# Kernel tuning notes

Measured on AMD Instinct MI355X. Metric: run time of the kernel, lower is better.

The kernel has to match this reference:

```python
import jax, jax.numpy as jnp
import numpy as np

N_NODES = 50000
N_EDGES = 400000
IN_CH = 7
EMBED = 128
EDGE_DIM = 6


def setup_inputs() -> dict:
    key = jax.random.key(0)
    ks = jax.random.split(key, 10)
    x = jax.random.normal(ks[0], (N_NODES, IN_CH), dtype=jnp.float32)
    edge_index = jax.random.randint(ks[1], (2, N_EDGES), 0, N_NODES, dtype=jnp.int64)
    edge_attr = jax.random.normal(ks[2], (N_EDGES, EDGE_DIM), dtype=jnp.float32)
    # edge MLP params: Linear(6,128) -> GELU -> Linear(128, 7*128)
    s1 = 1.0 / np.sqrt(EDGE_DIM)
    s2 = 1.0 / np.sqrt(EMBED)
    W1 = jax.random.uniform(ks[3], (EDGE_DIM, EMBED), jnp.float32, -s1, s1)
    b1 = jax.random.uniform(ks[4], (EMBED,), jnp.float32, -s1, s1)
    W2 = jax.random.uniform(ks[5], (EMBED, IN_CH * EMBED), jnp.float32, -s2, s2)
    b2 = jax.random.uniform(ks[6], (IN_CH * EMBED,), jnp.float32, -s2, s2)
    # NNConv root weight and bias
    s3 = 1.0 / np.sqrt(IN_CH)
    root = jax.random.uniform(ks[7], (IN_CH, EMBED), jnp.float32, -s3, s3)
    bias = jnp.zeros((EMBED,), dtype=jnp.float32)
    return {"x": x, "edge_index": edge_index, "edge_attr": edge_attr,
            "W1": W1, "b1": b1, "W2": W2, "b2": b2, "root": root, "bias": bias}


def reference(x, edge_index, edge_attr, W1, b1, W2, b2, root, bias):
    N = x.shape[0]
    src, dst = edge_index[0], edge_index[1]
    # edge MLP -> per-edge weight matrix [E, in_ch, embed]
    h = jax.nn.gelu(edge_attr @ W1 + b1, approximate=False)
    w = (h @ W2 + b2).reshape(-1, IN_CH, EMBED)
    # gather source node features, per-edge small matmul
    msg = jnp.einsum('ei,eio->eo', x[src], w)  # [E, embed]
    # mean aggregation at target nodes
    summed = jax.ops.segment_sum(msg, dst, num_segments=N)
    cnt = jax.ops.segment_sum(jnp.ones((msg.shape[0],), msg.dtype), dst, num_segments=N)
    aggr = summed / jnp.clip(cnt, 1.0)[:, None]
    return aggr + x @ root + bias
```

## Files before the change

kernel.cpp:

```cpp
#include <hip/hip_runtime.h>
#include <stdint.h>

#define NNODES 50000
#define NEDGES 400000
#define EMB 128
#define KD 896
#define BM 128

typedef __attribute__((ext_vector_type(8))) short bf16x8;
typedef __attribute__((ext_vector_type(4))) float f32x4;

__device__ __forceinline__ short f2bf(float f) {
  union { float f; uint32_t u; } v; v.f = f;
  uint32_t r = v.u + 0x7FFFu + ((v.u >> 16) & 1u);
  return (short)(r >> 16);
}
__device__ __forceinline__ float bf2f(short s) {
  union { uint32_t u; float f; } v; v.u = ((uint32_t)(uint16_t)s) << 16;
  return v.f;
}
__device__ __forceinline__ float fast_gelu(float x) {
  float x2 = x * x;
  float y = x * (0.7978845608f + 0.03567740814f * x2);
  float e = __expf(2.0f * y);
  float r = __builtin_amdgcn_rcpf(1.0f + e);
  return x - x * r;
}

__global__ void prep_B(const float* __restrict__ W2, short* __restrict__ Bp) {
  int idx = blockIdx.x * 256 + threadIdx.x;
  int m = idx & 7, l = (idx >> 3) & 63, c = idx >> 9;
  int sidx = c >> 2, wn = (c >> 1) & 1, f = c & 1;
  int p = sidx >> 2, kk = sidx & 3, i = p >> 1, fnh = p & 1;
  int o = (wn * 4 + fnh * 2 + f) * 16 + (l & 15);
  int k = kk * 32 + (l >> 4) * 8 + m;
  Bp[idx] = f2bf(W2[k * KD + i * EMB + o]);
}

__global__ void prep_W1(const float* __restrict__ W1f, const float* __restrict__ b1,
                        short* __restrict__ W1p) {
  int idx = blockIdx.x * 256 + threadIdx.x;
  int m = idx & 7, l = (idx >> 3) & 63, mt = idx >> 9;
  int o = mt * 16 + (l & 15), kseg = l >> 4;
  short v = 0;
  if (kseg < 2) {
    if (m < 6) v = f2bf(W1f[m * EMB + o]);
  } else if (kseg == 2) {
    if (m < 6) { float wv = W1f[m * EMB + o]; short hi = f2bf(wv); v = f2bf(wv - bf2f(hi)); }
  } else {
    if (m == 0) v = f2bf(b1[o]);
    else if (m == 1) { float bv = b1[o]; short hi = f2bf(bv); v = f2bf(bv - bf2f(hi)); }
  }
  W1p[idx] = v;
}

__global__ __launch_bounds__(256, 2)
void nnconv_main(const float* __restrict__ x,
                 const int* __restrict__ ei,
                 const float* __restrict__ ea,
                 const float* __restrict__ b2,
                 const short* __restrict__ Bp,
                 const short* __restrict__ W1p,
                 float* __restrict__ cnt,
                 float* __restrict__ out) {
  __shared__ __align__(16) short h_s[BM * EMB];
  __shared__ __align__(16) float x_t[7][132];
  __shared__ __align__(16) float ea_s[BM * 6];
  __shared__ int dst_s[BM];

  const int t = threadIdx.x;
  const int lane = t & 63;
  const int w = t >> 6;
  const int wm = w >> 1, wn = w & 1;
  const int rowA = lane & 15;
  const int kseg = lane >> 4;
  const int eb = blockIdx.x * BM;
  const char* BpB = (const char*)Bp + wn * 2048 + lane * 16;

  bf16x8 bcur[4][2];
#pragma unroll
  for (int kk = 0; kk < 4; ++kk)
#pragma unroll
    for (int f = 0; f < 2; ++f)
      bcur[kk][f] = *(const bf16x8*)(BpB + (((size_t)kk * 4 + f) << 10));

  if (t < 192)
    *(float4*)&ea_s[t * 4] = *(const float4*)&ea[(size_t)eb * 6 + t * 4];
  if (t < BM) {
    int s = ei[eb + t];
    int d = ei[NEDGES + eb + t];
    dst_s[t] = d;
#pragma unroll
    for (int i = 0; i < 7; ++i) x_t[i][t] = x[s * 7 + i];
    atomicAdd(&cnt[d], 1.0f);
  }
  __syncthreads();

  {
    bf16x8 wa[8];
#pragma unroll
    for (int mt = 0; mt < 8; ++mt)
      wa[mt] = *(const bf16x8*)(W1p + (mt * 64 + lane) * 8);
#pragma unroll
    for (int et2 = 0; et2 < 2; ++et2) {
      const int e = w * 32 + et2 * 16 + rowA;
      bf16x8 be = (bf16x8){0, 0, 0, 0, 0, 0, 0, 0};
      if (kseg == 3) {
        be[0] = f2bf(1.0f); be[1] = f2bf(1.0f);
      } else {
#pragma unroll
        for (int q = 0; q < 6; ++q) {
          float v = ea_s[e * 6 + q];
          short hi = f2bf(v);
          be[q] = (kseg == 1) ? f2bf(v - bf2f(hi)) : hi;
        }
      }
      const int swz = (e & 15) << 4;
#pragma unroll
      for (int mt = 0; mt < 8; ++mt) {
        f32x4 d = __builtin_amdgcn_mfma_f32_16x16x32_bf16(
            wa[mt], be, (f32x4){0.f, 0.f, 0.f, 0.f}, 0, 0, 0);
        uint32_t h0 = (uint16_t)f2bf(fast_gelu(d[0]));
        uint32_t h1 = (uint16_t)f2bf(fast_gelu(d[1]));
        uint32_t h2 = (uint16_t)f2bf(fast_gelu(d[2]));
        uint32_t h3 = (uint16_t)f2bf(fast_gelu(d[3]));
        uint2 u; u.x = h0 | (h1 << 16); u.y = h2 | (h3 << 16);
        int off = (mt * 32 + kseg * 8) ^ swz;
        *(uint2*)((char*)h_s + e * 256 + off) = u;
      }
    }
  }
  __syncthreads();

  bf16x8 A[4][4];
#pragma unroll
  for (int kk = 0; kk < 4; ++kk)
#pragma unroll
    for (int fm = 0; fm < 4; ++fm) {
      int row = wm * 64 + fm * 16 + rowA;
      int off = (kk * 64 + kseg * 16) ^ (rowA << 4);
      A[kk][fm] = *(const bf16x8*)((const char*)h_s + row * 256 + off);
    }

#pragma unroll
  for (int fh = 0; fh < 2; ++fh) {
    f32x4 acc2[4][2];
#pragma unroll
    for (int a = 0; a < 4; ++a) {
      acc2[a][0] = (f32x4){0.f, 0.f, 0.f, 0.f};
      acc2[a][1] = (f32x4){0.f, 0.f, 0.f, 0.f};
    }
#pragma unroll 1
    for (int i = 0; i < 7; ++i) {
      float b2v0 = b2[i * EMB + wn * 64 + fh * 32 + rowA];
      float b2v1 = b2[i * EMB + wn * 64 + fh * 32 + 16 + rowA];
      int nsidx;
      if (fh == 0) nsidx = (i < 6) ? (i + 1) * 8 : 4;
      else         nsidx = (i < 6) ? (i + 1) * 8 + 4 : 52;

      f32x4 tmp[4][2];
      const f32x4 zz = (f32x4){0.f, 0.f, 0.f, 0.f};
#pragma unroll
      for (int fm = 0; fm < 4; ++fm) {
        tmp[fm][0] = __builtin_amdgcn_mfma_f32_16x16x32_bf16(A[0][fm], bcur[0][0], zz, 0, 0, 0);
        tmp[fm][1] = __builtin_amdgcn_mfma_f32_16x16x32_bf16(A[0][fm], bcur[0][1], zz, 0, 0, 0);
      }
      bcur[0][0] = *(const bf16x8*)(BpB + (((size_t)(nsidx + 0) * 4 + 0) << 10));
      bcur[0][1] = *(const bf16x8*)(BpB + (((size_t)(nsidx + 0) * 4 + 1) << 10));
#pragma unroll
      for (int kk = 1; kk < 4; ++kk) {
#pragma unroll
        for (int fm = 0; fm < 4; ++fm) {
          tmp[fm][0] = __builtin_amdgcn_mfma_f32_16x16x32_bf16(A[kk][fm], bcur[kk][0], tmp[fm][0], 0, 0, 0);
          tmp[fm][1] = __builtin_amdgcn_mfma_f32_16x16x32_bf16(A[kk][fm], bcur[kk][1], tmp[fm][1], 0, 0, 0);
        }
        bcur[kk][0] = *(const bf16x8*)(BpB + (((size_t)(nsidx + kk) * 4 + 0) << 10));
        bcur[kk][1] = *(const bf16x8*)(BpB + (((size_t)(nsidx + kk) * 4 + 1) << 10));
      }
#pragma unroll
      for (int fm = 0; fm < 4; ++fm) {
        f32x4 xv = *(const f32x4*)&x_t[i][wm * 64 + fm * 16 + kseg * 4];
#pragma unroll
        for (int r = 0; r < 4; ++r) {
          acc2[fm][0][r] += xv[r] * (tmp[fm][0][r] + b2v0);
          acc2[fm][1][r] += xv[r] * (tmp[fm][1][r] + b2v1);
        }
      }
    }
#pragma unroll
    for (int fm = 0; fm < 4; ++fm)
#pragma unroll
      for (int r = 0; r < 4; ++r) {
        const int row = wm * 64 + fm * 16 + kseg * 4 + r;
        const int d = dst_s[row];
        float* op = out + (size_t)d * EMB + wn * 64 + fh * 32 + rowA;
        atomicAdd(op, acc2[fm][0][r]);
        atomicAdd(op + 16, acc2[fm][1][r]);
      }
  }
}

__global__ void finalize(const float* __restrict__ x, const float* __restrict__ root,
                         const float* __restrict__ bias, const float* __restrict__ cnt,
                         float* __restrict__ out) {
  int idx = blockIdx.x * 256 + threadIdx.x;
  int n = idx >> 7, o = idx & 127;
  float c = fmaxf(cnt[n], 1.0f);
  float v = out[idx] / c + bias[o];
#pragma unroll
  for (int i = 0; i < 7; ++i) v += x[n * 7 + i] * root[i * EMB + o];
  out[idx] = v;
}

extern "C" void kernel_launch(void* const* d_in, const int* in_sizes, int n_in,
                              void* d_out, int out_size, void* d_ws, size_t ws_size,
                              hipStream_t stream) {
  const float* x    = (const float*)d_in[0];
  const int*   ei   = (const int*)d_in[1];
  const float* ea   = (const float*)d_in[2];
  const float* W1   = (const float*)d_in[3];
  const float* b1   = (const float*)d_in[4];
  const float* W2   = (const float*)d_in[5];
  const float* b2   = (const float*)d_in[6];
  const float* root = (const float*)d_in[7];
  const float* bias = (const float*)d_in[8];
  float* out = (float*)d_out;

  short* Bp  = (short*)d_ws;
  short* W1p = (short*)((char*)d_ws + 128 * KD * 2);
  float* cnt = (float*)((char*)d_ws + 128 * KD * 2 + 8192);

  hipMemsetAsync(out, 0, (size_t)NNODES * EMB * sizeof(float), stream);
  hipMemsetAsync(cnt, 0, (size_t)NNODES * sizeof(float), stream);
  prep_B<<<448, 256, 0, stream>>>(W2, Bp);
  prep_W1<<<16, 256, 0, stream>>>(W1, b1, W1p);
  nnconv_main<<<NEDGES / BM, 256, 0, stream>>>(x, ei, ea, b2, Bp, W1p, cnt, out);
  finalize<<<NNODES * EMB / 256, 256, 0, stream>>>(x, root, bias, cnt, out);
}
```

Before: 301.3 us.

## Sort edges by destination and reduce runs in LDS before output atomics

Adds a counting sort of edges by destination node (histogram, single-block scan, scatter) so each main-kernel tile processes edges grouped by destination. Per-edge messages are staged in shared memory and each wave sums consecutive same-destination rows, issuing a plain store for runs fully inside its 32-row segment and an atomic only at segment boundaries. This cuts global float atomics roughly by the average in-degree. The cost is three extra kernel launches, a serial single-block scan, an extra LDS round trip, and gathered (uncoalesced) edge_attr and edge_index reads through the permutation.

```diff
diff --git a/kernel.cpp b/kernel.cpp
--- a/kernel.cpp
+++ b/kernel.cpp
@@ -54,6 +54,40 @@
   W1p[idx] = v;
 }
 
+__global__ void hist_dst(const int* __restrict__ ei, unsigned* __restrict__ cnt) {
+  int e = blockIdx.x * 256 + threadIdx.x;
+  if (e < NEDGES) atomicAdd(&cnt[ei[NEDGES + e]], 1u);
+}
+
+__global__ __launch_bounds__(1024)
+void scan_off(const unsigned* __restrict__ cnt, unsigned* __restrict__ woff) {
+  __shared__ unsigned ps[1024];
+  const int t = threadIdx.x;
+  const int lo = t * 49;
+  const int hi = (lo + 49 < NNODES) ? lo + 49 : NNODES;
+  unsigned s = 0;
+  for (int j = lo; j < hi; ++j) s += cnt[j];
+  ps[t] = s;
+  __syncthreads();
+  for (int d = 1; d < 1024; d <<= 1) {
+    unsigned v = (t >= d) ? ps[t - d] : 0u;
+    __syncthreads();
+    ps[t] += v;
+    __syncthreads();
+  }
+  unsigned run = (t > 0) ? ps[t - 1] : 0u;
+  for (int j = lo; j < hi; ++j) { woff[j] = run; run += cnt[j]; }
+}
+
+__global__ void scatter_e(const int* __restrict__ ei, unsigned* __restrict__ woff,
+                          unsigned* __restrict__ eord) {
+  int e = blockIdx.x * 256 + threadIdx.x;
+  if (e < NEDGES) {
+    unsigned p = atomicAdd(&woff[ei[NEDGES + e]], 1u);
+    eord[p] = (unsigned)e;
+  }
+}
+
 __global__ __launch_bounds__(256, 2)
 void nnconv_main(const float* __restrict__ x,
                  const int* __restrict__ ei,
@@ -61,12 +95,14 @@
                  const float* __restrict__ b2,
                  const short* __restrict__ Bp,
                  const short* __restrict__ W1p,
-                 float* __restrict__ cnt,
+                 const unsigned* __restrict__ eord,
                  float* __restrict__ out) {
-  __shared__ __align__(16) short h_s[BM * EMB];
+  __shared__ __align__(16) char smem[33280];
+  short* h_s = (short*)smem;
+  float* red_s = (float*)smem;
   __shared__ __align__(16) float x_t[7][132];
   __shared__ __align__(16) float ea_s[BM * 6];
-  __shared__ int dst_s[BM];
+  __shared__ int dst_s[BM + 4];
 
   const int t = threadIdx.x;
   const int lane = t & 63;
@@ -84,16 +120,17 @@
     for (int f = 0; f < 2; ++f)
       bcur[kk][f] = *(const bf16x8*)(BpB + (((size_t)kk * 4 + f) << 10));
 
-  if (t < 192)
-    *(float4*)&ea_s[t * 4] = *(const float4*)&ea[(size_t)eb * 6 + t * 4];
   if (t < BM) {
-    int s = ei[eb + t];
-    int d = ei[NEDGES + eb + t];
+    const int e = (int)eord[eb + t];
+    const int s = ei[e];
+    const int d = ei[NEDGES + e];
     dst_s[t] = d;
 #pragma unroll
     for (int i = 0; i < 7; ++i) x_t[i][t] = x[s * 7 + i];
-    atomicAdd(&cnt[d], 1.0f);
-  }
+#pragma unroll
+    for (int q = 0; q < 6; ++q) ea_s[t * 6 + q] = ea[(size_t)e * 6 + q];
+  }
+  if (t == BM) dst_s[BM] = -1;
   __syncthreads();
 
   {
@@ -187,25 +224,44 @@
         }
       }
     }
+
+    __syncthreads();
 #pragma unroll
     for (int fm = 0; fm < 4; ++fm)
 #pragma unroll
       for (int r = 0; r < 4; ++r) {
         const int row = wm * 64 + fm * 16 + kseg * 4 + r;
-        const int d = dst_s[row];
-        float* op = out + (size_t)d * EMB + wn * 64 + fh * 32 + rowA;
-        atomicAdd(op, acc2[fm][0][r]);
-        atomicAdd(op + 16, acc2[fm][1][r]);
-      }
+        red_s[row * 65 + wn * 32 + rowA]      = acc2[fm][0][r];
+        red_s[row * 65 + wn * 32 + 16 + rowA] = acc2[fm][1][r];
+      }
+    __syncthreads();
+    {
+      const int gcol = fh * 32 + (lane & 31) + (lane >> 5) * 64;
+      const int base = w * 32;
+      float run = 0.f;
+      int runstart = 0;
+      for (int j = 0; j < 32; ++j) {
+        run += red_s[(base + j) * 65 + lane];
+        const int d = dst_s[base + j];
+        const bool endrun = (j == 31) || (dst_s[base + j + 1] != d);
+        if (endrun) {
+          float* op = out + (size_t)d * EMB + gcol;
+          if (runstart > 0 && j < 31) *op = run;
+          else atomicAdd(op, run);
+          run = 0.f;
+          runstart = j + 1;
+        }
+      }
+    }
   }
 }
 
 __global__ void finalize(const float* __restrict__ x, const float* __restrict__ root,
-                         const float* __restrict__ bias, const float* __restrict__ cnt,
+                         const float* __restrict__ bias, const unsigned* __restrict__ cnt,
                          float* __restrict__ out) {
   int idx = blockIdx.x * 256 + threadIdx.x;
   int n = idx >> 7, o = idx & 127;
-  float c = fmaxf(cnt[n], 1.0f);
+  float c = fmaxf((float)cnt[n], 1.0f);
   float v = out[idx] / c + bias[o];
 #pragma unroll
   for (int i = 0; i < 7; ++i) v += x[n * 7 + i] * root[i * EMB + o];
@@ -226,14 +282,19 @@
   const float* bias = (const float*)d_in[8];
   float* out = (float*)d_out;
 
-  short* Bp  = (short*)d_ws;
-  short* W1p = (short*)((char*)d_ws + 128 * KD * 2);
-  float* cnt = (float*)((char*)d_ws + 128 * KD * 2 + 8192);
+  short*    Bp    = (short*)d_ws;
+  short*    W1p   = (short*)((char*)d_ws + 229376);
+  unsigned* cnt_u = (unsigned*)((char*)d_ws + 237568);
+  unsigned* woff  = (unsigned*)((char*)d_ws + 437568);
+  unsigned* eord  = (unsigned*)((char*)d_ws + 637568);
 
   hipMemsetAsync(out, 0, (size_t)NNODES * EMB * sizeof(float), stream);
-  hipMemsetAsync(cnt, 0, (size_t)NNODES * sizeof(float), stream);
+  hipMemsetAsync(cnt_u, 0, (size_t)NNODES * sizeof(unsigned), stream);
   prep_B<<<448, 256, 0, stream>>>(W2, Bp);
   prep_W1<<<16, 256, 0, stream>>>(W1, b1, W1p);
-  nnconv_main<<<NEDGES / BM, 256, 0, stream>>>(x, ei, ea, b2, Bp, W1p, cnt, out);
-  finalize<<<NNODES * EMB / 256, 256, 0, stream>>>(x, root, bias, cnt, out);
-}
+  hist_dst<<<(NEDGES + 255) / 256, 256, 0, stream>>>(ei, cnt_u);
+  scan_off<<<1, 1024, 0, stream>>>(cnt_u, woff);
+  scatter_e<<<(NEDGES + 255) / 256, 256, 0, stream>>>(ei, woff, eord);
+  nnconv_main<<<NEDGES / BM, 256, 0, stream>>>(x, ei, ea, b2, Bp, W1p, eord, out);
+  finalize<<<NNODES * EMB / 256, 256, 0, stream>>>(x, root, bias, cnt_u, out);
+}
```

New measurement: 355.8 us. +18.1%, slower.

## Sort edges by destination and reduce runs before scattering atomics

Applied to the files above, without the earlier changes.

Adds a counting sort of edges by destination: a histogram, a three-kernel prefix scan and a scatter. The main kernel then processes edges in sorted order, stages accumulators through shared memory, and sums runs of equal destinations so most output writes become plain stores. The b2 bias term is factored out through per-node sums of source features and applied in finalize. The main loop also double-buffers the W2 fragment loads. This targets the cost of 128 float atomics per edge, at the price of several extra small kernels, added atomics in the histogram, and an indirect gather of edge attributes.

```diff
diff --git a/kernel.cpp b/kernel.cpp
--- a/kernel.cpp
+++ b/kernel.cpp
@@ -54,19 +54,77 @@
   W1p[idx] = v;
 }
 
+__global__ void hist_dst(const int* __restrict__ ei, const float* __restrict__ x,
+                         unsigned* __restrict__ cnt, float* __restrict__ xsum) {
+  int e = blockIdx.x * 256 + threadIdx.x;
+  if (e < NEDGES) {
+    int d = ei[NEDGES + e];
+    int s = ei[e];
+    atomicAdd(&cnt[d], 1u);
+#pragma unroll
+    for (int i = 0; i < 7; ++i) atomicAdd(&xsum[d * 8 + i], x[s * 7 + i]);
+  }
+}
+
+__global__ void scanA(const unsigned* __restrict__ cnt, unsigned* __restrict__ woff,
+                      unsigned* __restrict__ part) {
+  __shared__ unsigned ps[256];
+  int t = threadIdx.x, n = blockIdx.x * 256 + t;
+  unsigned v = (n < NNODES) ? cnt[n] : 0u;
+  ps[t] = v; __syncthreads();
+  for (int d = 1; d < 256; d <<= 1) {
+    unsigned u = (t >= d) ? ps[t - d] : 0u;
+    __syncthreads(); ps[t] += u; __syncthreads();
+  }
+  if (n < NNODES) woff[n] = ps[t] - v;
+  if (t == 255) part[blockIdx.x] = ps[t];
+}
+
+__global__ void scanB(unsigned* __restrict__ part) {
+  __shared__ unsigned ps[256];
+  int t = threadIdx.x;
+  unsigned v = (t < 196) ? part[t] : 0u;
+  ps[t] = v; __syncthreads();
+  for (int d = 1; d < 256; d <<= 1) {
+    unsigned u = (t >= d) ? ps[t - d] : 0u;
+    __syncthreads(); ps[t] += u; __syncthreads();
+  }
+  if (t < 196) part[t] = ps[t] - v;
+}
+
+__global__ void scanC(unsigned* __restrict__ woff, const unsigned* __restrict__ part) {
+  int n = blockIdx.x * 256 + threadIdx.x;
+  if (n < NNODES) woff[n] += part[blockIdx.x];
+}
+
+__global__ void scatter_e(const int* __restrict__ ei, unsigned* __restrict__ woff,
+                          unsigned* __restrict__ eord, int* __restrict__ dsts,
+                          int* __restrict__ srcs) {
+  int e = blockIdx.x * 256 + threadIdx.x;
+  if (e < NEDGES) {
+    int d = ei[NEDGES + e];
+    unsigned p = atomicAdd(&woff[d], 1u);
+    eord[p] = (unsigned)e;
+    dsts[p] = d;
+    srcs[p] = ei[e];
+  }
+}
+
 __global__ __launch_bounds__(256, 2)
 void nnconv_main(const float* __restrict__ x,
-                 const int* __restrict__ ei,
                  const float* __restrict__ ea,
-                 const float* __restrict__ b2,
                  const short* __restrict__ Bp,
                  const short* __restrict__ W1p,
-                 float* __restrict__ cnt,
+                 const unsigned* __restrict__ eord,
+                 const int* __restrict__ dsts,
+                 const int* __restrict__ srcs,
                  float* __restrict__ out) {
-  __shared__ __align__(16) short h_s[BM * EMB];
+  __shared__ __align__(16) char smem[33280];
+  short* h_s = (short*)smem;
+  float* red_s = (float*)smem;
   __shared__ __align__(16) float x_t[7][132];
   __shared__ __align__(16) float ea_s[BM * 6];
-  __shared__ int dst_s[BM];
+  __shared__ int dst_s[BM + 4];
 
   const int t = threadIdx.x;
   const int lane = t & 63;
@@ -77,23 +135,23 @@
   const int eb = blockIdx.x * BM;
   const char* BpB = (const char*)Bp + wn * 2048 + lane * 16;
 
-  bf16x8 bcur[4][2];
+  bf16x8 bufA[4][2], bufB[4][2];
 #pragma unroll
   for (int kk = 0; kk < 4; ++kk)
 #pragma unroll
     for (int f = 0; f < 2; ++f)
-      bcur[kk][f] = *(const bf16x8*)(BpB + (((size_t)kk * 4 + f) << 10));
-
-  if (t < 192)
-    *(float4*)&ea_s[t * 4] = *(const float4*)&ea[(size_t)eb * 6 + t * 4];
+      bufA[kk][f] = *(const bf16x8*)(BpB + (((size_t)kk * 4 + f) << 10));
+
   if (t < BM) {
-    int s = ei[eb + t];
-    int d = ei[NEDGES + eb + t];
-    dst_s[t] = d;
+    const int s = srcs[eb + t];
+    dst_s[t] = dsts[eb + t];
 #pragma unroll
     for (int i = 0; i < 7; ++i) x_t[i][t] = x[s * 7 + i];
-    atomicAdd(&cnt[d], 1.0f);
-  }
+    const int e = (int)eord[eb + t];
+#pragma unroll
+    for (int q = 0; q < 6; ++q) ea_s[t * 6 + q] = ea[(size_t)e * 6 + q];
+  }
+  if (t == BM) dst_s[BM] = -1;
   __syncthreads();
 
   {
@@ -142,71 +200,109 @@
       A[kk][fm] = *(const bf16x8*)((const char*)h_s + row * 256 + off);
     }
 
-#pragma unroll
-  for (int fh = 0; fh < 2; ++fh) {
-    f32x4 acc2[4][2];
-#pragma unroll
-    for (int a = 0; a < 4; ++a) {
-      acc2[a][0] = (f32x4){0.f, 0.f, 0.f, 0.f};
-      acc2[a][1] = (f32x4){0.f, 0.f, 0.f, 0.f};
-    }
-#pragma unroll 1
-    for (int i = 0; i < 7; ++i) {
-      float b2v0 = b2[i * EMB + wn * 64 + fh * 32 + rowA];
-      float b2v1 = b2[i * EMB + wn * 64 + fh * 32 + 16 + rowA];
-      int nsidx;
-      if (fh == 0) nsidx = (i < 6) ? (i + 1) * 8 : 4;
-      else         nsidx = (i < 6) ? (i + 1) * 8 + 4 : 52;
-
-      f32x4 tmp[4][2];
-      const f32x4 zz = (f32x4){0.f, 0.f, 0.f, 0.f};
-#pragma unroll
-      for (int fm = 0; fm < 4; ++fm) {
-        tmp[fm][0] = __builtin_amdgcn_mfma_f32_16x16x32_bf16(A[0][fm], bcur[0][0], zz, 0, 0, 0);
-        tmp[fm][1] = __builtin_amdgcn_mfma_f32_16x16x32_bf16(A[0][fm], bcur[0][1], zz, 0, 0, 0);
-      }
-      bcur[0][0] = *(const bf16x8*)(BpB + (((size_t)(nsidx + 0) * 4 + 0) << 10));
-      bcur[0][1] = *(const bf16x8*)(BpB + (((size_t)(nsidx + 0) * 4 + 1) << 10));
-#pragma unroll
-      for (int kk = 1; kk < 4; ++kk) {
-#pragma unroll
-        for (int fm = 0; fm < 4; ++fm) {
-          tmp[fm][0] = __builtin_amdgcn_mfma_f32_16x16x32_bf16(A[kk][fm], bcur[kk][0], tmp[fm][0], 0, 0, 0);
-          tmp[fm][1] = __builtin_amdgcn_mfma_f32_16x16x32_bf16(A[kk][fm], bcur[kk][1], tmp[fm][1], 0, 0, 0);
-        }
-        bcur[kk][0] = *(const bf16x8*)(BpB + (((size_t)(nsidx + kk) * 4 + 0) << 10));
-        bcur[kk][1] = *(const bf16x8*)(BpB + (((size_t)(nsidx + kk) * 4 + 1) << 10));
-      }
-#pragma unroll
-      for (int fm = 0; fm < 4; ++fm) {
-        f32x4 xv = *(const f32x4*)&x_t[i][wm * 64 + fm * 16 + kseg * 4];
-#pragma unroll
-        for (int r = 0; r < 4; ++r) {
-          acc2[fm][0][r] += xv[r] * (tmp[fm][0][r] + b2v0);
-          acc2[fm][1][r] += xv[r] * (tmp[fm][1][r] + b2v1);
-        }
-      }
-    }
-#pragma unroll
-    for (int fm = 0; fm < 4; ++fm)
-#pragma unroll
-      for (int r = 0; r < 4; ++r) {
-        const int row = wm * 64 + fm * 16 + kseg * 4 + r;
-        const int d = dst_s[row];
-        float* op = out + (size_t)d * EMB + wn * 64 + fh * 32 + rowA;
-        atomicAdd(op, acc2[fm][0][r]);
-        atomicAdd(op + 16, acc2[fm][1][r]);
-      }
-  }
+#define ISTEP(BC, BN, NS, II)                                                        \
+  do {                                                                               \
+    _Pragma("unroll")                                                                \
+    for (int kk = 0; kk < 4; ++kk) {                                                 \
+      BN[kk][0] = *(const bf16x8*)(BpB + (((size_t)((NS) + kk) * 4 + 0) << 10));     \
+      BN[kk][1] = *(const bf16x8*)(BpB + (((size_t)((NS) + kk) * 4 + 1) << 10));     \
+    }                                                                                \
+    f32x4 tmp[4][2];                                                                 \
+    _Pragma("unroll")                                                                \
+    for (int a = 0; a < 4; ++a) {                                                    \
+      tmp[a][0] = (f32x4){0.f, 0.f, 0.f, 0.f};                                       \
+      tmp[a][1] = (f32x4){0.f, 0.f, 0.f, 0.f};                                       \
+    }                                                                                \
+    _Pragma("unroll")                                                                \
+    for (int kk = 0; kk < 4; ++kk)                                                   \
+      _Pragma("unroll")                                                              \
+      for (int fm = 0; fm < 4; ++fm) {                                               \
+        tmp[fm][0] = __builtin_amdgcn_mfma_f32_16x16x32_bf16(A[kk][fm], BC[kk][0],   \
+                                                             tmp[fm][0], 0, 0, 0);   \
+        tmp[fm][1] = __builtin_amdgcn_mfma_f32_16x16x32_bf16(A[kk][fm], BC[kk][1],   \
+                                                             tmp[fm][1], 0, 0, 0);   \
+      }                                                                              \
+    _Pragma("unroll")                                                                \
+    for (int fm = 0; fm < 4; ++fm) {                                                 \
+      f32x4 xv = *(const f32x4*)&x_t[II][wm * 64 + fm * 16 + kseg * 4];              \
+      _Pragma("unroll")                                                              \
+      for (int r = 0; r < 4; ++r) {                                                  \
+        acc2[fm][0][r] += xv[r] * tmp[fm][0][r];                                     \
+        acc2[fm][1][r] += xv[r] * tmp[fm][1][r];                                     \
+      }                                                                              \
+    }                                                                                \
+  } while (0)
+
+#define NS0(II) ((II) < 6 ? ((II) + 1) * 8 : 4)
+#define NS1(II) ((II) < 6 ? ((II) + 1) * 8 + 4 : 52)
+
+#define EPILOG(FH)                                                                   \
+  do {                                                                               \
+    __syncthreads();                                                                 \
+    _Pragma("unroll")                                                                \
+    for (int fm = 0; fm < 4; ++fm)                                                   \
+      _Pragma("unroll")                                                              \
+      for (int r = 0; r < 4; ++r) {                                                  \
+        const int row = wm * 64 + fm * 16 + kseg * 4 + r;                            \
+        red_s[row * 65 + wn * 32 + rowA]      = acc2[fm][0][r];                      \
+        red_s[row * 65 + wn * 32 + 16 + rowA] = acc2[fm][1][r];                      \
+      }                                                                              \
+    __syncthreads();                                                                 \
+    {                                                                                \
+      const int gcol = (FH) * 32 + (lane & 31) + (lane >> 5) * 64;                   \
+      const int base = w * 32;                                                       \
+      float run = 0.f;                                                               \
+      int runstart = 0;                                                              \
+      for (int j = 0; j < 32; ++j) {                                                 \
+        run += red_s[(base + j) * 65 + lane];                                        \
+        const int d = dst_s[base + j];                                               \
+        const bool endrun = (j == 31) || (dst_s[base + j + 1] != d);                 \
+        if (endrun) {                                                                \
+          float* op = out + (size_t)d * EMB + gcol;                                  \
+          if (runstart > 0 && j < 31) *op = run;                                     \
+          else atomicAdd(op, run);                                                   \
+          run = 0.f;                                                                 \
+          runstart = j + 1;                                                          \
+        }                                                                            \
+      }                                                                              \
+    }                                                                                \
+  } while (0)
+
+  f32x4 acc2[4][2];
+#pragma unroll
+  for (int a = 0; a < 4; ++a) { acc2[a][0] = (f32x4){0,0,0,0}; acc2[a][1] = (f32x4){0,0,0,0}; }
+  ISTEP(bufA, bufB, NS0(0), 0);
+  ISTEP(bufB, bufA, NS0(1), 1);
+  ISTEP(bufA, bufB, NS0(2), 2);
+  ISTEP(bufB, bufA, NS0(3), 3);
+  ISTEP(bufA, bufB, NS0(4), 4);
+  ISTEP(bufB, bufA, NS0(5), 5);
+  ISTEP(bufA, bufB, NS0(6), 6);
+  EPILOG(0);
+
+#pragma unroll
+  for (int a = 0; a < 4; ++a) { acc2[a][0] = (f32x4){0,0,0,0}; acc2[a][1] = (f32x4){0,0,0,0}; }
+  ISTEP(bufB, bufA, NS1(0), 0);
+  ISTEP(bufA, bufB, NS1(1), 1);
+  ISTEP(bufB, bufA, NS1(2), 2);
+  ISTEP(bufA, bufB, NS1(3), 3);
+  ISTEP(bufB, bufA, NS1(4), 4);
+  ISTEP(bufA, bufB, NS1(5), 5);
+  ISTEP(bufB, bufA, NS1(6), 6);
+  EPILOG(1);
 }
 
 __global__ void finalize(const float* __restrict__ x, const float* __restrict__ root,
-                         const float* __restrict__ bias, const float* __restrict__ cnt,
+                         const float* __restrict__ bias, const float* __restrict__ b2,
+                         const unsigned* __restrict__ cnt, const float* __restrict__ xsum,
                          float* __restrict__ out) {
   int idx = blockIdx.x * 256 + threadIdx.x;
   int n = idx >> 7, o = idx & 127;
-  float c = fmaxf(cnt[n], 1.0f);
-  float v = out[idx] / c + bias[o];
+  float c = fmaxf((float)cnt[n], 1.0f);
+  float s = out[idx];
+#pragma unroll
+  for (int i = 0; i < 7; ++i) s += xsum[n * 8 + i] * b2[i * EMB + o];
+  float v = s / c + bias[o];
 #pragma unroll
   for (int i = 0; i < 7; ++i) v += x[n * 7 + i] * root[i * EMB + o];
   out[idx] = v;
@@ -226,14 +322,26 @@
   const float* bias = (const float*)d_in[8];
   float* out = (float*)d_out;
 
-  short* Bp  = (short*)d_ws;
-  short* W1p = (short*)((char*)d_ws + 128 * KD * 2);
-  float* cnt = (float*)((char*)d_ws + 128 * KD * 2 + 8192);
+  char* ws = (char*)d_ws;
+  short*    Bp    = (short*)ws;
+  short*    W1p   = (short*)(ws + 229376);
+  unsigned* cnt_u = (unsigned*)(ws + 237568);
+  float*    xsum  = (float*)(ws + 437568);
+  unsigned* woff  = (unsigned*)(ws + 2037568);
+  unsigned* part  = (unsigned*)(ws + 2237568);
+  unsigned* eord  = (unsigned*)(ws + 2238592);
+  int*      dsts  = (int*)(ws + 3838592);
+  int*      srcs  = (int*)(ws + 5438592);
 
   hipMemsetAsync(out, 0, (size_t)NNODES * EMB * sizeof(float), stream);
-  hipMemsetAsync(cnt, 0, (size_t)NNODES * sizeof(float), stream);
+  hipMemsetAsync(cnt_u, 0, 1800000, stream);
   prep_B<<<448, 256, 0, stream>>>(W2, Bp);
   prep_W1<<<16, 256, 0, stream>>>(W1, b1, W1p);
-  nnconv_main<<<NEDGES / BM, 256, 0, stream>>>(x, ei, ea, b2, Bp, W1p, cnt, out);
-  finalize<<<NNODES * EMB / 256, 256, 0, stream>>>(x, root, bias, cnt, out);
-}
+  hist_dst<<<(NEDGES + 255) / 256, 256, 0, stream>>>(ei, x, cnt_u, xsum);
+  scanA<<<196, 256, 0, stream>>>(cnt_u, woff, part);
+  scanB<<<1, 256, 0, stream>>>(part);
+  scanC<<<196, 256, 0, stream>>>(woff, part);
+  scatter_e<<<(NEDGES + 255) / 256, 256, 0, stream>>>(ei, woff, eord, dsts, srcs);
+  nnconv_main<<<NEDGES / BM, 256, 0, stream>>>(x, ea, Bp, W1p, eord, dsts, srcs, out);
+  finalize<<<NNODES * EMB / 256, 256, 0, stream>>>(x, root, bias, b2, cnt_u, xsum, out);
+}
```

Result: slower. 434.3 us (+44.2%).
